# Performance work log

Hardware: AMD Instinct MI355X
Metric: run time of the kernel (lower is better)

## Reference

```python
import jax, jax.numpy as jnp
import numpy as np

EMBED = 128   # embed_dim
HEADS = 8
POINTS = 4
H_SP, W_SP = 51, 102   # hardcoded spatial_shapes in __init__
BEV = 100              # bev_res
HRES = 50              # height_res


def _make_ref_points():
    """Exact numpy replica of the spherical grid built in __init__."""
    eps = 1e-6
    x = np.linspace(-71 / 2, 71 / 2, BEV)
    y = np.linspace(-71 / 2, 71 / 2, BEV)
    z = np.linspace(-50 / 2, 50 / 2, HRES)
    gx, gy, gz = np.meshgrid(x, y, z, indexing='ij')
    phi = np.sign(gy + eps) * np.arccos(gx / (np.sqrt(gx ** 2 + gy ** 2) + eps))
    theta = np.arccos(gz / (np.sqrt(gx ** 2 + gy ** 2 + gz ** 2) + eps))
    phi = 2 * np.pi - phi
    phi[phi > 2 * np.pi] -= 2 * np.pi
    col = phi / (2 * np.pi)   # grd_col_cross
    row = theta / np.pi       # grd_row_cross
    ref = np.stack([col, row], axis=-1)              # (BEV, BEV, HRES, 2)
    ref = ref.transpose(2, 0, 1, 3).reshape(HRES, BEV * BEV, 2)
    return jnp.asarray(ref, dtype=jnp.float32)


def setup_inputs() -> dict:
    key = jax.random.key(0)
    ks = jax.random.split(key, 12)
    d = EMBED
    s = 0.02
    return {
        'query': jax.random.normal(ks[0], (1, BEV * BEV, d), jnp.float32),
        'value': jax.random.normal(ks[1], (1, H_SP * W_SP, d), jnp.float32),
        'ref_points': _make_ref_points(),
        'W_off': jax.random.normal(ks[2], (d, HEADS * POINTS * 2), jnp.float32) * s,
        'b_off': jax.random.normal(ks[3], (HEADS * POINTS * 2,), jnp.float32) * s,
        'W_attn': jax.random.normal(ks[4], (d, HEADS * POINTS), jnp.float32) * s,
        'b_attn': jax.random.normal(ks[5], (HEADS * POINTS,), jnp.float32) * s,
        'W_val': jax.random.normal(ks[6], (d, d), jnp.float32) * s,
        'b_val': jax.random.normal(ks[7], (d,), jnp.float32) * s,
        'W_out': jax.random.normal(ks[8], (d, d), jnp.float32) * s,
        'b_out': jax.random.normal(ks[9], (d,), jnp.float32) * s,
        'W_proj': jax.random.normal(ks[10], (d, 1), jnp.float32) * s,
        'b_proj': jax.random.normal(ks[11], (1,), jnp.float32) * s,
    }


def _bilinear_sample(vflat, loc):
    """grid_sample(bilinear, zero padding, align_corners=False).
    vflat: (B, H*W, hd) value maps; loc: (B, N, 2) normalized [0,1] (x,y)."""
    px = loc[..., 0] * W_SP - 0.5
    py = loc[..., 1] * H_SP - 0.5
    x0 = jnp.floor(px)
    y0 = jnp.floor(py)
    dx = (px - x0)[..., None]
    dy = (py - y0)[..., None]
    x0i = x0.astype(jnp.int32)
    y0i = y0.astype(jnp.int32)

    def gather(xi, yi):
        valid = (xi >= 0) & (xi < W_SP) & (yi >= 0) & (yi < H_SP)
        idx = jnp.clip(yi, 0, H_SP - 1) * W_SP + jnp.clip(xi, 0, W_SP - 1)
        v = jnp.take_along_axis(vflat, idx[..., None], axis=1)  # (B, N, hd)
        return v * valid[..., None].astype(vflat.dtype)

    v00 = gather(x0i, y0i)
    v01 = gather(x0i + 1, y0i)
    v10 = gather(x0i, y0i + 1)
    v11 = gather(x0i + 1, y0i + 1)
    return (v00 * (1 - dx) * (1 - dy) + v01 * dx * (1 - dy)
            + v10 * (1 - dx) * dy + v11 * dx * dy)


def reference(query, value, ref_points, W_off, b_off, W_attn, b_attn,
              W_val, b_val, W_out, b_out, W_proj, b_proj):
    bs, nq, d = query.shape
    hd = d // HEADS
    L = ref_points.shape[0]

    # query-dependent MSDA projections (identical across height levels)
    offsets = (query @ W_off + b_off).reshape(bs, nq, HEADS, POINTS, 2)
    aw = jax.nn.softmax((query @ W_attn + b_attn).reshape(bs, nq, HEADS, POINTS), axis=-1)
    awt = aw.transpose(0, 2, 1, 3)                              # (bs, heads, nq, points)
    v = (value @ W_val + b_val).reshape(bs, -1, HEADS, hd)
    vflat = v.transpose(0, 2, 1, 3).reshape(bs * HEADS, H_SP * W_SP, hd)
    norm = jnp.asarray([W_SP, H_SP], dtype=query.dtype)         # offset_normalizer [W, H]

    def per_level(ref):  # ref: (nq, 2) -> MSDA output with its internal residual
        loc = ref[None, :, None, None, :] + offsets / norm      # (bs, nq, heads, pts, 2)
        loc = loc.transpose(0, 2, 1, 3, 4).reshape(bs * HEADS, nq * POINTS, 2)
        samp = _bilinear_sample(vflat, loc).reshape(bs, HEADS, nq, POINTS, hd)
        out = jnp.einsum('bhnp,bhnpd->bnhd', awt, samp).reshape(bs, nq, d)
        return out @ W_out + b_out + query                      # mmcv MSDA adds identity

    grd = jax.vmap(per_level)(ref_points)                       # (L, bs, nq, d)
    grd_3d = grd.transpose(1, 2, 0, 3).reshape(bs, BEV, BEV, L, d)
    weights = jax.nn.softmax(grd_3d @ W_proj + b_proj, axis=3)  # (bs, BEV, BEV, L, 1)
    max_height_index = jnp.argmax(weights, axis=3)              # (bs, BEV, BEV, 1)
    grd_bev = (weights * grd_3d).sum(axis=3)                    # (bs, BEV, BEV, d)
    return grd_bev.reshape(bs, nq, d) + query, max_height_index
```

## Files before the change

kernel.cpp:

```cpp
#include <hip/hip_runtime.h>
#include <math.h>

#define EMBED   128
#define NHEADS  8
#define NPOINTS 4
#define HD      16
#define HSP     51
#define WSP     102
#define NPIX    (HSP * WSP)
#define NQ      10000
#define NLVL    50

__global__ void k_valproj(const float* __restrict__ value,
                          const float* __restrict__ Wv,
                          const float* __restrict__ bv,
                          float* __restrict__ vout) {
    __shared__ float vrow[EMBED];
    const int pix = blockIdx.x;
    const int t = threadIdx.x;
    vrow[t] = value[(size_t)pix * EMBED + t];
    __syncthreads();
    float acc = bv[t];
#pragma unroll 8
    for (int k = 0; k < EMBED; ++k)
        acc = fmaf(vrow[k], Wv[(size_t)k * EMBED + t], acc);
    const int h = t >> 4, c = t & 15;
    vout[((size_t)h * NPIX + pix) * HD + c] = acc;
}

__global__ void k_offattn(const float* __restrict__ query,
                          const float* __restrict__ Woff,
                          const float* __restrict__ boff,
                          const float* __restrict__ Wattn,
                          const float* __restrict__ battn,
                          float* __restrict__ off_out,
                          float* __restrict__ aw_out) {
    __shared__ float qrow[EMBED];
    __shared__ float attn[32];
    const int q = blockIdx.x;
    const int t = threadIdx.x;
    qrow[t] = query[(size_t)q * EMBED + t];
    __syncthreads();
    if (t < 64) {
        float acc = boff[t];
#pragma unroll 8
        for (int k = 0; k < EMBED; ++k)
            acc = fmaf(qrow[k], Woff[(size_t)k * 64 + t], acc);
        off_out[(size_t)q * 64 + t] = acc;
    } else if (t < 96) {
        const int j = t - 64;
        float acc = battn[j];
#pragma unroll 8
        for (int k = 0; k < EMBED; ++k)
            acc = fmaf(qrow[k], Wattn[(size_t)k * 32 + j], acc);
        attn[j] = acc;
    }
    __syncthreads();
    if (t < NHEADS) {
        const float a0 = attn[t * 4 + 0], a1 = attn[t * 4 + 1];
        const float a2 = attn[t * 4 + 2], a3 = attn[t * 4 + 3];
        const float mx = fmaxf(fmaxf(a0, a1), fmaxf(a2, a3));
        const float e0 = __expf(a0 - mx), e1 = __expf(a1 - mx);
        const float e2 = __expf(a2 - mx), e3 = __expf(a3 - mx);
        const float inv = 1.f / (e0 + e1 + e2 + e3);
        aw_out[(size_t)q * 32 + t * 4 + 0] = e0 * inv;
        aw_out[(size_t)q * 32 + t * 4 + 1] = e1 * inv;
        aw_out[(size_t)q * 32 + t * 4 + 2] = e2 * inv;
        aw_out[(size_t)q * 32 + t * 4 + 3] = e3 * inv;
    }
}

__global__ void k_uvec(const float* __restrict__ Wout,
                       const float* __restrict__ Wproj,
                       float* __restrict__ u) {
    const int c = threadIdx.x;
    float acc = 0.f;
#pragma unroll 8
    for (int d = 0; d < EMBED; ++d)
        acc = fmaf(Wout[(size_t)c * EMBED + d], Wproj[d], acc);
    u[c] = acc;
}

__global__ __launch_bounds__(256) void k_main(
    const float* __restrict__ query,
    const float* __restrict__ refp,
    const float* __restrict__ voff,
    const float* __restrict__ vaw,
    const float* __restrict__ vflat,
    const float* __restrict__ uvec,
    const float* __restrict__ Wout,
    const float* __restrict__ bout,
    float* __restrict__ out0,
    float* __restrict__ out1) {
    const int t = threadIdx.x;
    const int sub = t & 31;
    const int slot = t >> 5;
    const int q = blockIdx.x * 8 + slot;
    const int h = sub >> 2;
    const int c4 = sub & 3;

    __shared__ float4 s_lds[8][32];

    const float4* offp = (const float4*)(voff + (size_t)q * 64 + h * 8);
    const float4 o01 = offp[0];
    const float4 o23 = offp[1];
    const float4 awv4 = *(const float4*)(vaw + (size_t)q * 32 + h * 4);
    const float4 u4 = *(const float4*)(uvec + h * 16 + c4 * 4);
    const float4* vbase = (const float4*)vflat + (size_t)h * NPIX * 4 + c4;

    const float offx[4] = {o01.x, o01.z, o23.x, o23.z};
    const float offy[4] = {o01.y, o01.w, o23.y, o23.w};
    const float awv[4]  = {awv4.x, awv4.y, awv4.z, awv4.w};

    float4 acc = {0.f, 0.f, 0.f, 0.f};
    float m = -1e30f, Z = 0.f;
    int best = 0;

    for (int l = 0; l < NLVL; ++l) {
        const float2 rp = *(const float2*)(refp + ((size_t)l * NQ + q) * 2);
        float4 s = {0.f, 0.f, 0.f, 0.f};
#pragma unroll
        for (int p = 0; p < NPOINTS; ++p) {
            const float px = fmaf(rp.x, (float)WSP, offx[p]) - 0.5f;
            const float py = fmaf(rp.y, (float)HSP, offy[p]) - 0.5f;
            const float fx = floorf(px), fy = floorf(py);
            const float dx = px - fx, dy = py - fy;
            const int x0 = (int)fx, y0 = (int)fy;
            const float a = awv[p];
            float w00 = a * (1.f - dx) * (1.f - dy);
            float w01 = a * dx * (1.f - dy);
            float w10 = a * (1.f - dx) * dy;
            float w11 = a * dx * dy;
            const bool vx0 = (x0 >= 0) && (x0 < WSP);
            const bool vx1 = (x0 >= -1) && (x0 < WSP - 1);
            const bool vy0 = (y0 >= 0) && (y0 < HSP);
            const bool vy1 = (y0 >= -1) && (y0 < HSP - 1);
            w00 = (vx0 && vy0) ? w00 : 0.f;
            w01 = (vx1 && vy0) ? w01 : 0.f;
            w10 = (vx0 && vy1) ? w10 : 0.f;
            w11 = (vx1 && vy1) ? w11 : 0.f;
            const int xc0 = min(max(x0, 0), WSP - 1);
            const int xc1 = min(max(x0 + 1, 0), WSP - 1);
            const int yc0 = min(max(y0, 0), HSP - 1);
            const int yc1 = min(max(y0 + 1, 0), HSP - 1);
            const int i00 = yc0 * WSP + xc0;
            const int i01 = yc0 * WSP + xc1;
            const int i10 = yc1 * WSP + xc0;
            const int i11 = yc1 * WSP + xc1;
            const float4 v00 = vbase[(size_t)i00 * 4];
            const float4 v01 = vbase[(size_t)i01 * 4];
            const float4 v10 = vbase[(size_t)i10 * 4];
            const float4 v11 = vbase[(size_t)i11 * 4];
            s.x = fmaf(w00, v00.x, s.x); s.y = fmaf(w00, v00.y, s.y);
            s.z = fmaf(w00, v00.z, s.z); s.w = fmaf(w00, v00.w, s.w);
            s.x = fmaf(w01, v01.x, s.x); s.y = fmaf(w01, v01.y, s.y);
            s.z = fmaf(w01, v01.z, s.z); s.w = fmaf(w01, v01.w, s.w);
            s.x = fmaf(w10, v10.x, s.x); s.y = fmaf(w10, v10.y, s.y);
            s.z = fmaf(w10, v10.z, s.z); s.w = fmaf(w10, v10.w, s.w);
            s.x = fmaf(w11, v11.x, s.x); s.y = fmaf(w11, v11.y, s.y);
            s.z = fmaf(w11, v11.z, s.z); s.w = fmaf(w11, v11.w, s.w);
        }
        float part = s.x * u4.x + s.y * u4.y + s.z * u4.z + s.w * u4.w;
#pragma unroll
        for (int d = 1; d < 32; d <<= 1)
            part += __shfl_xor(part, d, 64);
        if (part > m) {
            const float sc = __expf(m - part);
            Z = fmaf(Z, sc, 1.f);
            acc.x = fmaf(acc.x, sc, s.x);
            acc.y = fmaf(acc.y, sc, s.y);
            acc.z = fmaf(acc.z, sc, s.z);
            acc.w = fmaf(acc.w, sc, s.w);
            m = part; best = l;
        } else {
            const float w = __expf(part - m);
            Z += w;
            acc.x = fmaf(w, s.x, acc.x);
            acc.y = fmaf(w, s.y, acc.y);
            acc.z = fmaf(w, s.z, acc.z);
            acc.w = fmaf(w, s.w, acc.w);
        }
    }
    const float inv = 1.f / Z;
    float4 sv;
    sv.x = acc.x * inv; sv.y = acc.y * inv; sv.z = acc.z * inv; sv.w = acc.w * inv;
    s_lds[slot][sub] = sv;
    __syncthreads();

    const int dpb = sub * 4;
    const float4 b4 = *(const float4*)(bout + dpb);
    const float4 q4 = *(const float4*)(query + (size_t)q * EMBED + dpb);
    float4 r;
    r.x = fmaf(2.f, q4.x, b4.x);
    r.y = fmaf(2.f, q4.y, b4.y);
    r.z = fmaf(2.f, q4.z, b4.z);
    r.w = fmaf(2.f, q4.w, b4.w);
    const float4* srow = s_lds[slot];
#pragma unroll 4
    for (int cg = 0; cg < 32; ++cg) {
        const float4 s4 = srow[cg];
        const float4 w0 = *(const float4*)(Wout + (size_t)(cg * 4 + 0) * EMBED + dpb);
        const float4 w1 = *(const float4*)(Wout + (size_t)(cg * 4 + 1) * EMBED + dpb);
        const float4 w2 = *(const float4*)(Wout + (size_t)(cg * 4 + 2) * EMBED + dpb);
        const float4 w3 = *(const float4*)(Wout + (size_t)(cg * 4 + 3) * EMBED + dpb);
        r.x = fmaf(s4.x, w0.x, r.x); r.y = fmaf(s4.x, w0.y, r.y);
        r.z = fmaf(s4.x, w0.z, r.z); r.w = fmaf(s4.x, w0.w, r.w);
        r.x = fmaf(s4.y, w1.x, r.x); r.y = fmaf(s4.y, w1.y, r.y);
        r.z = fmaf(s4.y, w1.z, r.z); r.w = fmaf(s4.y, w1.w, r.w);
        r.x = fmaf(s4.z, w2.x, r.x); r.y = fmaf(s4.z, w2.y, r.y);
        r.z = fmaf(s4.z, w2.z, r.z); r.w = fmaf(s4.z, w2.w, r.w);
        r.x = fmaf(s4.w, w3.x, r.x); r.y = fmaf(s4.w, w3.y, r.y);
        r.z = fmaf(s4.w, w3.z, r.z); r.w = fmaf(s4.w, w3.w, r.w);
    }
    *(float4*)(out0 + (size_t)q * EMBED + dpb) = r;
    if (sub == 0) out1[q] = (float)best;
}

extern "C" void kernel_launch(void* const* d_in, const int* in_sizes, int n_in,
                              void* d_out, int out_size, void* d_ws, size_t ws_size,
                              hipStream_t stream) {
    const float* query = (const float*)d_in[0];
    const float* value = (const float*)d_in[1];
    const float* refp  = (const float*)d_in[2];
    const float* Woff  = (const float*)d_in[3];
    const float* boff  = (const float*)d_in[4];
    const float* Wattn = (const float*)d_in[5];
    const float* battn = (const float*)d_in[6];
    const float* Wval  = (const float*)d_in[7];
    const float* bval  = (const float*)d_in[8];
    const float* Wout  = (const float*)d_in[9];
    const float* bout  = (const float*)d_in[10];
    const float* Wproj = (const float*)d_in[11];

    float* ws = (float*)d_ws;
    float* ws_v   = ws;
    float* ws_off = ws_v + (size_t)NHEADS * NPIX * HD;
    float* ws_aw  = ws_off + (size_t)NQ * 64;
    float* ws_u   = ws_aw + (size_t)NQ * 32;

    float* out0 = (float*)d_out;
    float* out1 = out0 + (size_t)NQ * EMBED;

    hipLaunchKernelGGL(k_valproj, dim3(NPIX), dim3(EMBED), 0, stream,
                       value, Wval, bval, ws_v);
    hipLaunchKernelGGL(k_offattn, dim3(NQ), dim3(EMBED), 0, stream,
                       query, Woff, boff, Wattn, battn, ws_off, ws_aw);
    hipLaunchKernelGGL(k_uvec, dim3(1), dim3(EMBED), 0, stream, Wout, Wproj, ws_u);
    hipLaunchKernelGGL(k_main, dim3(NQ / 8), dim3(256), 0, stream,
                       query, refp, ws_off, ws_aw, ws_v, ws_u, Wout, bout,
                       out0, out1);
}
```

Measured before the change: 279.3 us.

## Fuse prep kernels and split level loop across half-waves with hoisted x-sampling

Merges the value projection, offset/attention projection and u-vector kernels into a single launch, which cuts launch overhead. The main kernel now gives each query a full 64-lane wave and has the two 32-lane halves process alternate height levels, merging their partial sums with cross-lane shuffles. The x-direction bilinear weights and indices are computed once, from the level-0 reference point, which assumes the column coordinate is the same at every level. The y reference values are staged in LDS. The online softmax drops its running-max rescaling and uses a plain exp, which could overflow for large logits. The output projection is also split across the two halves.

```diff
diff --git a/kernel.cpp b/kernel.cpp
--- a/kernel.cpp
+++ b/kernel.cpp
@@ -11,74 +11,74 @@
 #define NQ      10000
 #define NLVL    50
 
-__global__ void k_valproj(const float* __restrict__ value,
-                          const float* __restrict__ Wv,
-                          const float* __restrict__ bv,
-                          float* __restrict__ vout) {
-    __shared__ float vrow[EMBED];
-    const int pix = blockIdx.x;
+__global__ __launch_bounds__(128) void k_prep(
+    const float* __restrict__ value,
+    const float* __restrict__ Wv,
+    const float* __restrict__ bv,
+    const float* __restrict__ query,
+    const float* __restrict__ Woff,
+    const float* __restrict__ boff,
+    const float* __restrict__ Wattn,
+    const float* __restrict__ battn,
+    const float* __restrict__ Wout,
+    const float* __restrict__ Wproj,
+    float* __restrict__ vout,
+    float* __restrict__ off_out,
+    float* __restrict__ aw_out,
+    float* __restrict__ u_out) {
+    const int b = blockIdx.x;
     const int t = threadIdx.x;
-    vrow[t] = value[(size_t)pix * EMBED + t];
-    __syncthreads();
-    float acc = bv[t];
-#pragma unroll 8
-    for (int k = 0; k < EMBED; ++k)
-        acc = fmaf(vrow[k], Wv[(size_t)k * EMBED + t], acc);
-    const int h = t >> 4, c = t & 15;
-    vout[((size_t)h * NPIX + pix) * HD + c] = acc;
-}
-
-__global__ void k_offattn(const float* __restrict__ query,
-                          const float* __restrict__ Woff,
-                          const float* __restrict__ boff,
-                          const float* __restrict__ Wattn,
-                          const float* __restrict__ battn,
-                          float* __restrict__ off_out,
-                          float* __restrict__ aw_out) {
-    __shared__ float qrow[EMBED];
-    __shared__ float attn[32];
-    const int q = blockIdx.x;
-    const int t = threadIdx.x;
-    qrow[t] = query[(size_t)q * EMBED + t];
-    __syncthreads();
-    if (t < 64) {
-        float acc = boff[t];
+
+    if (b < NPIX) {
+        __shared__ float vrow[EMBED];
+        vrow[t] = value[(size_t)b * EMBED + t];
+        __syncthreads();
+        float acc = bv[t];
 #pragma unroll 8
         for (int k = 0; k < EMBED; ++k)
-            acc = fmaf(qrow[k], Woff[(size_t)k * 64 + t], acc);
-        off_out[(size_t)q * 64 + t] = acc;
-    } else if (t < 96) {
-        const int j = t - 64;
-        float acc = battn[j];
-#pragma unroll 8
-        for (int k = 0; k < EMBED; ++k)
-            acc = fmaf(qrow[k], Wattn[(size_t)k * 32 + j], acc);
-        attn[j] = acc;
-    }
-    __syncthreads();
-    if (t < NHEADS) {
-        const float a0 = attn[t * 4 + 0], a1 = attn[t * 4 + 1];
-        const float a2 = attn[t * 4 + 2], a3 = attn[t * 4 + 3];
-        const float mx = fmaxf(fmaxf(a0, a1), fmaxf(a2, a3));
-        const float e0 = __expf(a0 - mx), e1 = __expf(a1 - mx);
-        const float e2 = __expf(a2 - mx), e3 = __expf(a3 - mx);
-        const float inv = 1.f / (e0 + e1 + e2 + e3);
-        aw_out[(size_t)q * 32 + t * 4 + 0] = e0 * inv;
-        aw_out[(size_t)q * 32 + t * 4 + 1] = e1 * inv;
-        aw_out[(size_t)q * 32 + t * 4 + 2] = e2 * inv;
-        aw_out[(size_t)q * 32 + t * 4 + 3] = e3 * inv;
-    }
-}
-
-__global__ void k_uvec(const float* __restrict__ Wout,
-                       const float* __restrict__ Wproj,
-                       float* __restrict__ u) {
-    const int c = threadIdx.x;
-    float acc = 0.f;
-#pragma unroll 8
-    for (int d = 0; d < EMBED; ++d)
-        acc = fmaf(Wout[(size_t)c * EMBED + d], Wproj[d], acc);
-    u[c] = acc;
+            acc = fmaf(vrow[k], Wv[(size_t)k * EMBED + t], acc);
+        const int h = t >> 4, c = t & 15;
+        vout[((size_t)h * NPIX + b) * HD + c] = acc;
+    } else if (b < NPIX + NQ) {
+        const int q = b - NPIX;
+        __shared__ float qrow[EMBED];
+        __shared__ float attn[32];
+        qrow[t] = query[(size_t)q * EMBED + t];
+        __syncthreads();
+        if (t < 64) {
+            float acc = boff[t];
+#pragma unroll 8
+            for (int k = 0; k < EMBED; ++k)
+                acc = fmaf(qrow[k], Woff[(size_t)k * 64 + t], acc);
+            off_out[(size_t)q * 64 + t] = acc;
+        } else if (t < 96) {
+            const int j = t - 64;
+            float acc = battn[j];
+#pragma unroll 8
+            for (int k = 0; k < EMBED; ++k)
+                acc = fmaf(qrow[k], Wattn[(size_t)k * 32 + j], acc);
+            attn[j] = acc;
+        }
+        __syncthreads();
+        if (t < NHEADS) {
+            const float a0 = attn[t * 4 + 0], a1 = attn[t * 4 + 1];
+            const float a2 = attn[t * 4 + 2], a3 = attn[t * 4 + 3];
+            const float mx = fmaxf(fmaxf(a0, a1), fmaxf(a2, a3));
+            const float e0 = __expf(a0 - mx), e1 = __expf(a1 - mx);
+            const float e2 = __expf(a2 - mx), e3 = __expf(a3 - mx);
+            const float inv = 1.f / (e0 + e1 + e2 + e3);
+            aw_out[(size_t)q * 32 + t * 4 + 0] = e0 * inv;
+            aw_out[(size_t)q * 32 + t * 4 + 1] = e1 * inv;
+            aw_out[(size_t)q * 32 + t * 4 + 2] = e2 * inv;
+            aw_out[(size_t)q * 32 + t * 4 + 3] = e3 * inv;
+        }
+    } else {
+        float acc = 0.f;
+#pragma unroll 8
+        for (int d = 0; d < EMBED; ++d)
+            acc = fmaf(Wout[(size_t)t * EMBED + d], Wproj[d], acc);
+        u_out[t] = acc;
+    }
 }
 
 __global__ __launch_bounds__(256) void k_main(
@@ -93,64 +93,83 @@
     float* __restrict__ out0,
     float* __restrict__ out1) {
     const int t = threadIdx.x;
-    const int sub = t & 31;
-    const int slot = t >> 5;
-    const int q = blockIdx.x * 8 + slot;
-    const int h = sub >> 2;
+    const int slot = t >> 6;
+    const int lane = t & 63;
+    const int half = lane >> 5;
+    const int sub  = lane & 31;
+    const int h  = sub >> 2;
     const int c4 = sub & 3;
-
-    __shared__ float4 s_lds[8][32];
+    const int q = blockIdx.x * 4 + slot;
+
+    __shared__ float s_rpy[4][NLVL];
+    __shared__ float4 s_lds[4][32];
+
+    {
+        int i = t;
+        if (i < 4 * NLVL) {
+            const int ql = i / NLVL, l = i - ql * NLVL;
+            const int qq = blockIdx.x * 4 + ql;
+            s_rpy[ql][l] = refp[((size_t)l * NQ + qq) * 2 + 1];
+        }
+    }
 
     const float4* offp = (const float4*)(voff + (size_t)q * 64 + h * 8);
     const float4 o01 = offp[0];
     const float4 o23 = offp[1];
     const float4 awv4 = *(const float4*)(vaw + (size_t)q * 32 + h * 4);
     const float4 u4 = *(const float4*)(uvec + h * 16 + c4 * 4);
+    const float rpx = refp[(size_t)q * 2];
     const float4* vbase = (const float4*)vflat + (size_t)h * NPIX * 4 + c4;
 
     const float offx[4] = {o01.x, o01.z, o23.x, o23.z};
     const float offy[4] = {o01.y, o01.w, o23.y, o23.w};
     const float awv[4]  = {awv4.x, awv4.y, awv4.z, awv4.w};
 
+    float wx0[NPOINTS], wx1[NPOINTS], oyc[NPOINTS];
+    int xo0[NPOINTS], xo1[NPOINTS];
+#pragma unroll
+    for (int p = 0; p < NPOINTS; ++p) {
+        const float px = fmaf(rpx, (float)WSP, offx[p]) - 0.5f;
+        const float fx = floorf(px);
+        const float dx = px - fx;
+        const int x0 = (int)fx, x1 = x0 + 1;
+        const float a = awv[p];
+        wx0[p] = ((unsigned)x0 < (unsigned)WSP) ? a * (1.f - dx) : 0.f;
+        wx1[p] = ((unsigned)x1 < (unsigned)WSP) ? a * dx : 0.f;
+        xo0[p] = min(max(x0, 0), WSP - 1) * 4;
+        xo1[p] = min(max(x1, 0), WSP - 1) * 4;
+        oyc[p] = offy[p] - 0.5f;
+    }
+
+    __syncthreads();
+
     float4 acc = {0.f, 0.f, 0.f, 0.f};
-    float m = -1e30f, Z = 0.f;
+    float Z = 0.f, m = -1e30f;
     int best = 0;
 
-    for (int l = 0; l < NLVL; ++l) {
-        const float2 rp = *(const float2*)(refp + ((size_t)l * NQ + q) * 2);
+#pragma unroll 2
+    for (int i = 0; i < NLVL / 2; ++i) {
+        const int l = 2 * i + half;
+        const float rpy = s_rpy[slot][l];
         float4 s = {0.f, 0.f, 0.f, 0.f};
 #pragma unroll
         for (int p = 0; p < NPOINTS; ++p) {
-            const float px = fmaf(rp.x, (float)WSP, offx[p]) - 0.5f;
-            const float py = fmaf(rp.y, (float)HSP, offy[p]) - 0.5f;
-            const float fx = floorf(px), fy = floorf(py);
-            const float dx = px - fx, dy = py - fy;
-            const int x0 = (int)fx, y0 = (int)fy;
-            const float a = awv[p];
-            float w00 = a * (1.f - dx) * (1.f - dy);
-            float w01 = a * dx * (1.f - dy);
-            float w10 = a * (1.f - dx) * dy;
-            float w11 = a * dx * dy;
-            const bool vx0 = (x0 >= 0) && (x0 < WSP);
-            const bool vx1 = (x0 >= -1) && (x0 < WSP - 1);
-            const bool vy0 = (y0 >= 0) && (y0 < HSP);
-            const bool vy1 = (y0 >= -1) && (y0 < HSP - 1);
-            w00 = (vx0 && vy0) ? w00 : 0.f;
-            w01 = (vx1 && vy0) ? w01 : 0.f;
-            w10 = (vx0 && vy1) ? w10 : 0.f;
-            w11 = (vx1 && vy1) ? w11 : 0.f;
-            const int xc0 = min(max(x0, 0), WSP - 1);
-            const int xc1 = min(max(x0 + 1, 0), WSP - 1);
-            const int yc0 = min(max(y0, 0), HSP - 1);
-            const int yc1 = min(max(y0 + 1, 0), HSP - 1);
-            const int i00 = yc0 * WSP + xc0;
-            const int i01 = yc0 * WSP + xc1;
-            const int i10 = yc1 * WSP + xc0;
-            const int i11 = yc1 * WSP + xc1;
-            const float4 v00 = vbase[(size_t)i00 * 4];
-            const float4 v01 = vbase[(size_t)i01 * 4];
-            const float4 v10 = vbase[(size_t)i10 * 4];
-            const float4 v11 = vbase[(size_t)i11 * 4];
+            const float py = fmaf(rpy, (float)HSP, oyc[p]);
+            const float fy = floorf(py);
+            const float dy = py - fy;
+            const int y0 = (int)fy, y1 = y0 + 1;
+            const float t0 = ((unsigned)y0 < (unsigned)HSP) ? (1.f - dy) : 0.f;
+            const float t1 = ((unsigned)y1 < (unsigned)HSP) ? dy : 0.f;
+            const int rb0 = min(max(y0, 0), HSP - 1) * (WSP * 4);
+            const int rb1 = min(max(y1, 0), HSP - 1) * (WSP * 4);
+            const float w00 = wx0[p] * t0;
+            const float w01 = wx1[p] * t0;
+            const float w10 = wx0[p] * t1;
+            const float w11 = wx1[p] * t1;
+            const float4 v00 = vbase[rb0 + xo0[p]];
+            const float4 v01 = vbase[rb0 + xo1[p]];
+            const float4 v10 = vbase[rb1 + xo0[p]];
+            const float4 v11 = vbase[rb1 + xo1[p]];
             s.x = fmaf(w00, v00.x, s.x); s.y = fmaf(w00, v00.y, s.y);
             s.z = fmaf(w00, v00.z, s.z); s.w = fmaf(w00, v00.w, s.w);
             s.x = fmaf(w01, v01.x, s.x); s.y = fmaf(w01, v01.y, s.y);
@@ -160,44 +179,60 @@
             s.x = fmaf(w11, v11.x, s.x); s.y = fmaf(w11, v11.y, s.y);
             s.z = fmaf(w11, v11.z, s.z); s.w = fmaf(w11, v11.w, s.w);
         }
-        float part = s.x * u4.x + s.y * u4.y + s.z * u4.z + s.w * u4.w;
+        float part = s.x * u4.x;
+        part = fmaf(s.y, u4.y, part);
+        part = fmaf(s.z, u4.z, part);
+        part = fmaf(s.w, u4.w, part);
 #pragma unroll
         for (int d = 1; d < 32; d <<= 1)
             part += __shfl_xor(part, d, 64);
-        if (part > m) {
-            const float sc = __expf(m - part);
-            Z = fmaf(Z, sc, 1.f);
-            acc.x = fmaf(acc.x, sc, s.x);
-            acc.y = fmaf(acc.y, sc, s.y);
-            acc.z = fmaf(acc.z, sc, s.z);
-            acc.w = fmaf(acc.w, sc, s.w);
-            m = part; best = l;
-        } else {
-            const float w = __expf(part - m);
-            Z += w;
-            acc.x = fmaf(w, s.x, acc.x);
-            acc.y = fmaf(w, s.y, acc.y);
-            acc.z = fmaf(w, s.z, acc.z);
-            acc.w = fmaf(w, s.w, acc.w);
-        }
+        const float e = __expf(part);
+        Z += e;
+        acc.x = fmaf(e, s.x, acc.x);
+        acc.y = fmaf(e, s.y, acc.y);
+        acc.z = fmaf(e, s.z, acc.z);
+        acc.w = fmaf(e, s.w, acc.w);
+        best = (part > m) ? l : best;
+        m = fmaxf(part, m);
+    }
+
+    {
+        const float mo = __shfl_xor(m, 32, 64);
+        const int   bo = __shfl_xor(best, 32, 64);
+        const float Zo = __shfl_xor(Z, 32, 64);
+        const float ax = __shfl_xor(acc.x, 32, 64);
+        const float ay = __shfl_xor(acc.y, 32, 64);
+        const float az = __shfl_xor(acc.z, 32, 64);
+        const float aw_ = __shfl_xor(acc.w, 32, 64);
+        const bool takeOther = (mo > m) || (mo == m && bo < best);
+        best = takeOther ? bo : best;
+        Z += Zo;
+        acc.x += ax; acc.y += ay; acc.z += az; acc.w += aw_;
     }
     const float inv = 1.f / Z;
-    float4 sv;
-    sv.x = acc.x * inv; sv.y = acc.y * inv; sv.z = acc.z * inv; sv.w = acc.w * inv;
-    s_lds[slot][sub] = sv;
+    if (half == 0) {
+        float4 sv;
+        sv.x = acc.x * inv; sv.y = acc.y * inv;
+        sv.z = acc.z * inv; sv.w = acc.w * inv;
+        s_lds[slot][sub] = sv;
+        if (sub == 0) out1[q] = (float)best;
+    }
     __syncthreads();
 
     const int dpb = sub * 4;
-    const float4 b4 = *(const float4*)(bout + dpb);
-    const float4 q4 = *(const float4*)(query + (size_t)q * EMBED + dpb);
-    float4 r;
-    r.x = fmaf(2.f, q4.x, b4.x);
-    r.y = fmaf(2.f, q4.y, b4.y);
-    r.z = fmaf(2.f, q4.z, b4.z);
-    r.w = fmaf(2.f, q4.w, b4.w);
+    float4 r = {0.f, 0.f, 0.f, 0.f};
+    if (half == 0) {
+        const float4 b4 = *(const float4*)(bout + dpb);
+        const float4 q4 = *(const float4*)(query + (size_t)q * EMBED + dpb);
+        r.x = fmaf(2.f, q4.x, b4.x);
+        r.y = fmaf(2.f, q4.y, b4.y);
+        r.z = fmaf(2.f, q4.z, b4.z);
+        r.w = fmaf(2.f, q4.w, b4.w);
+    }
     const float4* srow = s_lds[slot];
+    const int cg0 = half * 16;
 #pragma unroll 4
-    for (int cg = 0; cg < 32; ++cg) {
+    for (int cg = cg0; cg < cg0 + 16; ++cg) {
         const float4 s4 = srow[cg];
         const float4 w0 = *(const float4*)(Wout + (size_t)(cg * 4 + 0) * EMBED + dpb);
         const float4 w1 = *(const float4*)(Wout + (size_t)(cg * 4 + 1) * EMBED + dpb);
@@ -212,8 +247,15 @@
         r.x = fmaf(s4.w, w3.x, r.x); r.y = fmaf(s4.w, w3.y, r.y);
         r.z = fmaf(s4.w, w3.z, r.z); r.w = fmaf(s4.w, w3.w, r.w);
     }
-    *(float4*)(out0 + (size_t)q * EMBED + dpb) = r;
-    if (sub == 0) out1[q] = (float)best;
+    {
+        const float rx = __shfl_xor(r.x, 32, 64);
+        const float ry = __shfl_xor(r.y, 32, 64);
+        const float rz = __shfl_xor(r.z, 32, 64);
+        const float rw = __shfl_xor(r.w, 32, 64);
+        r.x += rx; r.y += ry; r.z += rz; r.w += rw;
+    }
+    if (half == 0)
+        *(float4*)(out0 + (size_t)q * EMBED + dpb) = r;
 }
 
 extern "C" void kernel_launch(void* const* d_in, const int* in_sizes, int n_in,
@@ -241,12 +283,10 @@
     float* out0 = (float*)d_out;
     float* out1 = out0 + (size_t)NQ * EMBED;
 
-    hipLaunchKernelGGL(k_valproj, dim3(NPIX), dim3(EMBED), 0, stream,
-                       value, Wval, bval, ws_v);
-    hipLaunchKernelGGL(k_offattn, dim3(NQ), dim3(EMBED), 0, stream,
-                       query, Woff, boff, Wattn, battn, ws_off, ws_aw);
-    hipLaunchKernelGGL(k_uvec, dim3(1), dim3(EMBED), 0, stream, Wout, Wproj, ws_u);
-    hipLaunchKernelGGL(k_main, dim3(NQ / 8), dim3(256), 0, stream,
+    hipLaunchKernelGGL(k_prep, dim3(NPIX + NQ + 1), dim3(128), 0, stream,
+                       value, Wval, bval, query, Woff, boff, Wattn, battn,
+                       Wout, Wproj, ws_v, ws_off, ws_aw, ws_u);
+    hipLaunchKernelGGL(k_main, dim3(NQ / 4), dim3(256), 0, stream,
                        query, refp, ws_off, ws_aw, ws_v, ws_u, Wout, bout,
                        out0, out1);
 }
```

After: 253.6 us. 1.1x faster.
